# Optimization experiments

Measured on AMD Instinct MI355X. Metric: run time of the kernel, lower is better.

The kernel has to match this reference:

```python
import jax, jax.numpy as jnp
import numpy as np

RAD2DEG = 180.0 / 3.14159  # module uses 3.14159, not pi

def _conv2d(x, w):
    # x: (N,1,H,W), w: (O,1,3,3), SAME padding, stride 1
    return jax.lax.conv_general_dilated(
        x, w, window_strides=(1, 1), padding='SAME',
        dimension_numbers=('NCHW', 'OIHW', 'NCHW'))

def _make_filters():
    sobel = np.array([[1, 0, -1], [2, 0, -2], [1, 0, -1]], dtype=np.float32)
    f0   = [[0,0,0],[0,1,-1],[0,0,0]]
    f45  = [[0,0,0],[0,1,0],[0,0,-1]]
    f90  = [[0,0,0],[0,1,0],[0,-1,0]]
    f135 = [[0,0,0],[0,1,0],[-1,0,0]]
    f180 = [[0,0,0],[-1,1,0],[0,0,0]]
    f225 = [[-1,0,0],[0,1,0],[0,0,0]]
    f270 = [[0,-1,0],[0,1,0],[0,0,0]]
    f315 = [[0,0,-1],[0,1,0],[0,0,0]]
    dirs = np.stack([f0,f45,f90,f135,f180,f225,f270,f315]).astype(np.float32)
    return sobel, dirs

def setup_inputs() -> dict:
    key = jax.random.key(0)
    H, W = 2160, 3840
    img = jax.random.uniform(key, (1, 3, H, W), dtype=jnp.float32)
    sobel, dirs = _make_filters()
    sobel_h = jnp.asarray(sobel)[None, None]          # (1,1,3,3)
    sobel_v = jnp.asarray(sobel.T)[None, None]        # (1,1,3,3)
    dir_w = jnp.asarray(dirs)[:, None]                # (8,1,3,3)
    return {"img": img, "sobel_h": sobel_h, "sobel_v": sobel_v, "dir_w": dir_w}

def reference(img, sobel_h, sobel_v, dir_w):
    # grayscale: mean of the 3 channels
    gray = (img[:, 0:1] + img[:, 1:2] + img[:, 2:3]) / 3.0        # (1,1,H,W)
    grad_x = _conv2d(gray, sobel_h)
    grad_y = _conv2d(gray, sobel_v)
    grad_mag = jnp.sqrt(grad_x ** 2 + grad_y ** 2)                # (1,1,H,W)
    # orientation in degrees, snapped to multiples of 45 (round-half-even, like torch.round)
    ori = jnp.round((jnp.arctan2(grad_y, grad_x) * RAD2DEG + 180.0) / 45.0)
    idx_pos = jnp.mod(ori, 8.0).astype(jnp.int32)                 # (1,1,H,W)
    idx_neg = jnp.mod(ori + 4.0, 8.0).astype(jnp.int32)
    all_filtered = _conv2d(grad_mag, dir_w)                       # (1,8,H,W)
    # per-pixel channel select (the flattened gather in the original)
    pos = jnp.take_along_axis(all_filtered, idx_pos, axis=1)      # (1,1,H,W)
    neg = jnp.take_along_axis(all_filtered, idx_neg, axis=1)
    is_max = jnp.minimum(pos, neg) > 0.0
    # in-place aliasing in the original: thin_edges/early_threshold alias grad_mag,
    # so the final binary map is: is_max AND (grad_mag >= 0.2)
    th = jnp.where(is_max & (grad_mag >= 0.2), 1.0, 0.0).astype(jnp.float32)
    return th
```

## Files before the change

kernel.cpp:

```cpp
#include <hip/hip_runtime.h>
#include <math.h>

#define IMG_W 3840
#define IMG_H 2160
#define TW 128
#define TH 16

#define DXPACK 0x901A
#define DYPACK 0x1A9

#define T1_SLOPE 0.41421317376456f
#define T2_SLOPE 2.41420676743300f
#define SECT_EPS 3.0e-5f

__device__ __forceinline__ int slow_sector(float sx, float sy) {
#pragma clang fp contract(off)
    const float RADF = (float)(180.0 / 3.14159);
    float t = atan2f(sy, sx);
    float wv = ((t * RADF) + 180.0f) / 45.0f;
    float ori = rintf(wv);
    float fr = fabsf(wv - ori);
    if (fr > 0.4995f) {
        double td = atan2((double)sy, (double)sx);
        float t2 = (float)td;
        wv = ((t2 * RADF) + 180.0f) / 45.0f;
        ori = rintf(wv);
    }
    return ((int)ori) & 7;
}

__global__ __launch_bounds__(256) void canny_like_kernel(const float* __restrict__ img,
                                                         float* __restrict__ out) {
#pragma clang fp contract(off)
    __shared__ float lds_g[TH + 4][TW + 4];
    __shared__ float lds_m[TH + 2][TW + 2];

    const int tx = threadIdx.x;
    const int ty = threadIdx.y;
    const int tid = ty * TW + tx;
    const int x0 = blockIdx.x * TW;
    const int y0 = blockIdx.y * TH;

    for (int i = tid; i < (TH + 4) * (TW + 4); i += 256) {
        int ry = i / (TW + 4);
        int rx = i - ry * (TW + 4);
        int gyy = y0 - 2 + ry;
        int gxx = x0 - 2 + rx;
        float v = 0.0f;
        if (gyy >= 0 && gyy < IMG_H && gxx >= 0 && gxx < IMG_W) {
            int base = gyy * IMG_W + gxx;
            float c0 = img[base];
            float c1 = img[base + IMG_H * IMG_W];
            float c2 = img[base + 2 * IMG_H * IMG_W];
            v = ((c0 + c1) + c2) / 3.0f;
        }
        lds_g[ry][rx] = v;
    }
    __syncthreads();

    for (int i = tid; i < (TH + 2) * (TW + 2); i += 256) {
        int my = i / (TW + 2);
        int mx = i - my * (TW + 2);
        int gyy = y0 - 1 + my;
        int gxx = x0 - 1 + mx;
        float v = 0.0f;
        if (gyy >= 0 && gyy < IMG_H && gxx >= 0 && gxx < IMG_W) {
            float a00 = lds_g[my][mx],     a01 = lds_g[my][mx + 1],     a02 = lds_g[my][mx + 2];
            float a10 = lds_g[my + 1][mx],                              a12 = lds_g[my + 1][mx + 2];
            float a20 = lds_g[my + 2][mx], a21 = lds_g[my + 2][mx + 1], a22 = lds_g[my + 2][mx + 2];
            float sx = a00;
            sx = sx - a02;
            sx = sx + 2.0f * a10;
            sx = sx - 2.0f * a12;
            sx = sx + a20;
            sx = sx - a22;
            float sy = a00;
            sy = sy + 2.0f * a01;
            sy = sy + a02;
            sy = sy - a20;
            sy = sy - 2.0f * a21;
            sy = sy - a22;
            v = sqrtf(sx * sx + sy * sy);
        }
        lds_m[my][mx] = v;
    }
    __syncthreads();

    for (int r = 0; r < TH / 2; ++r) {
        int oy = r * 2 + ty;
        int my = oy + 1, mx = tx + 1;
        int ry = oy + 2, rx = tx + 2;
        float a00 = lds_g[ry - 1][rx - 1], a01 = lds_g[ry - 1][rx], a02 = lds_g[ry - 1][rx + 1];
        float a10 = lds_g[ry][rx - 1],                              a12 = lds_g[ry][rx + 1];
        float a20 = lds_g[ry + 1][rx - 1], a21 = lds_g[ry + 1][rx], a22 = lds_g[ry + 1][rx + 1];
        float sx = a00;
        sx = sx - a02;
        sx = sx + 2.0f * a10;
        sx = sx - 2.0f * a12;
        sx = sx + a20;
        sx = sx - a22;
        float sy = a00;
        sy = sy + 2.0f * a01;
        sy = sy + a02;
        sy = sy - a20;
        sy = sy - 2.0f * a21;
        sy = sy - a22;

        float ax = fabsf(sx), ay = fabsf(sy);
        float d1 = ay - T1_SLOPE * ax;
        float d2 = ay - T2_SLOPE * ax;
        float s = ax + ay;
        int idx;
        if (fabsf(d1) < SECT_EPS * s || fabsf(d2) < SECT_EPS * s) {
            idx = slow_sector(sx, sy);
        } else if (d1 < 0.0f) {
            idx = (sx > 0.0f) ? 4 : 0;
        } else if (d2 > 0.0f) {
            idx = (sy > 0.0f) ? 6 : 2;
        } else {
            idx = (sx > 0.0f) ? ((sy > 0.0f) ? 5 : 3)
                              : ((sy > 0.0f) ? 7 : 1);
        }
        int dxo = ((DXPACK >> (2 * idx)) & 3) - 1;
        int dyo = ((DYPACK >> (2 * idx)) & 3) - 1;

        float mc = lds_m[my][mx];
        float pos = mc - lds_m[my + dyo][mx + dxo];
        float neg = mc - lds_m[my - dyo][mx - dxo];
        float res = (fminf(pos, neg) > 0.0f && mc >= 0.2f) ? 1.0f : 0.0f;
        out[(y0 + oy) * IMG_W + (x0 + tx)] = res;
    }
}

extern "C" void kernel_launch(void* const* d_in, const int* in_sizes, int n_in,
                              void* d_out, int out_size, void* d_ws, size_t ws_size,
                              hipStream_t stream) {
    const float* img = (const float*)d_in[0];
    float* out = (float*)d_out;
    dim3 grid(IMG_W / TW, IMG_H / TH);
    dim3 block(TW, 2);
    canny_like_kernel<<<grid, block, 0, stream>>>(img, out);
}
```

Baseline: 178.5 us.

## Use overlapping tiles, compute orientation once per halo pixel, store neighbor offsets in LDS

Each block now loads a 128-wide tile that overlaps its neighbours by the halo and writes only the 124 inner output columns. Staging loops therefore map one thread to one column with no integer division. The gradient direction is computed once alongside the magnitude and stored as a packed LDS offset, so the final pass no longer recomputes the Sobel and reads neighbours through a single offset. slow_sector is marked noinline to keep register pressure down. In exchange, some halo work is redundant, the grid grows (31 column tiles with a partial last tile), and the final pass leaves a few lanes idle.

```diff
diff --git a/kernel.cpp b/kernel.cpp
--- a/kernel.cpp
+++ b/kernel.cpp
@@ -3,8 +3,11 @@
 
 #define IMG_W 3840
 #define IMG_H 2160
-#define TW 128
+#define TW 124
 #define TH 16
+#define LW 128
+#define GROWS (TH + 4)
+#define MROWS (TH + 2)
 
 #define DXPACK 0x901A
 #define DYPACK 0x1A9
@@ -13,7 +16,7 @@
 #define T2_SLOPE 2.41420676743300f
 #define SECT_EPS 3.0e-5f
 
-__device__ __forceinline__ int slow_sector(float sx, float sy) {
+__device__ __noinline__ int slow_sector(float sx, float sy) {
 #pragma clang fp contract(off)
     const float RADF = (float)(180.0 / 3.14159);
     float t = atan2f(sy, sx);
@@ -32,103 +35,88 @@
 __global__ __launch_bounds__(256) void canny_like_kernel(const float* __restrict__ img,
                                                          float* __restrict__ out) {
 #pragma clang fp contract(off)
-    __shared__ float lds_g[TH + 4][TW + 4];
-    __shared__ float lds_m[TH + 2][TW + 2];
+    __shared__ float lds_g[GROWS][LW];
+    __shared__ float lds_m[MROWS][LW];
+    __shared__ short lds_o[MROWS][LW];
 
-    const int tx = threadIdx.x;
-    const int ty = threadIdx.y;
-    const int tid = ty * TW + tx;
-    const int x0 = blockIdx.x * TW;
-    const int y0 = blockIdx.y * TH;
+    const int c = threadIdx.x;
+    const int h = threadIdx.y;
+    const int gx = blockIdx.x * TW - 2 + c;
+    const int gy0 = blockIdx.y * TH - 2;
+    const bool xok = (unsigned)gx < (unsigned)IMG_W;
 
-    for (int i = tid; i < (TH + 4) * (TW + 4); i += 256) {
-        int ry = i / (TW + 4);
-        int rx = i - ry * (TW + 4);
-        int gyy = y0 - 2 + ry;
-        int gxx = x0 - 2 + rx;
+    const float* p = img + gx;
+    for (int i = 0; i < GROWS / 2; ++i) {
+        int gy = gy0 + 2 * i + h;
         float v = 0.0f;
-        if (gyy >= 0 && gyy < IMG_H && gxx >= 0 && gxx < IMG_W) {
-            int base = gyy * IMG_W + gxx;
-            float c0 = img[base];
-            float c1 = img[base + IMG_H * IMG_W];
-            float c2 = img[base + 2 * IMG_H * IMG_W];
+        if (xok && (unsigned)gy < (unsigned)IMG_H) {
+            long o = (long)gy * IMG_W;
+            float c0 = p[o];
+            float c1 = p[o + (long)IMG_W * IMG_H];
+            float c2 = p[o + 2l * IMG_W * IMG_H];
             v = ((c0 + c1) + c2) / 3.0f;
         }
-        lds_g[ry][rx] = v;
+        lds_g[2 * i + h][c] = v;
     }
     __syncthreads();
 
-    for (int i = tid; i < (TH + 2) * (TW + 2); i += 256) {
-        int my = i / (TW + 2);
-        int mx = i - my * (TW + 2);
-        int gyy = y0 - 1 + my;
-        int gxx = x0 - 1 + mx;
-        float v = 0.0f;
-        if (gyy >= 0 && gyy < IMG_H && gxx >= 0 && gxx < IMG_W) {
-            float a00 = lds_g[my][mx],     a01 = lds_g[my][mx + 1],     a02 = lds_g[my][mx + 2];
-            float a10 = lds_g[my + 1][mx],                              a12 = lds_g[my + 1][mx + 2];
-            float a20 = lds_g[my + 2][mx], a21 = lds_g[my + 2][mx + 1], a22 = lds_g[my + 2][mx + 2];
-            float sx = a00;
-            sx = sx - a02;
-            sx = sx + 2.0f * a10;
-            sx = sx - 2.0f * a12;
-            sx = sx + a20;
-            sx = sx - a22;
-            float sy = a00;
-            sy = sy + 2.0f * a01;
-            sy = sy + a02;
-            sy = sy - a20;
-            sy = sy - 2.0f * a21;
-            sy = sy - a22;
-            v = sqrtf(sx * sx + sy * sy);
+    if (c >= 1 && c <= 126) {
+        for (int i = 0; i < MROWS / 2; ++i) {
+            int r = 2 * i + h;
+            int gy = gy0 + 1 + r;
+            float mag = 0.0f;
+            short offp = 0;
+            if (xok && (unsigned)gy < (unsigned)IMG_H) {
+                float a00 = lds_g[r][c - 1],     a01 = lds_g[r][c],     a02 = lds_g[r][c + 1];
+                float a10 = lds_g[r + 1][c - 1],                        a12 = lds_g[r + 1][c + 1];
+                float a20 = lds_g[r + 2][c - 1], a21 = lds_g[r + 2][c], a22 = lds_g[r + 2][c + 1];
+                float sx = a00;
+                sx = sx - a02;
+                sx = sx + 2.0f * a10;
+                sx = sx - 2.0f * a12;
+                sx = sx + a20;
+                sx = sx - a22;
+                float sy = a00;
+                sy = sy + 2.0f * a01;
+                sy = sy + a02;
+                sy = sy - a20;
+                sy = sy - 2.0f * a21;
+                sy = sy - a22;
+                mag = sqrtf(sx * sx + sy * sy);
+
+                float ax = fabsf(sx), ay = fabsf(sy);
+                float d1 = fmaf(-T1_SLOPE, ax, ay);
+                float d2 = fmaf(-T2_SLOPE, ax, ay);
+                float s = ax + ay;
+                int dxo, dyo;
+                if (fabsf(d1) < SECT_EPS * s || fabsf(d2) < SECT_EPS * s) {
+                    int idx = slow_sector(sx, sy);
+                    dxo = ((DXPACK >> (2 * idx)) & 3) - 1;
+                    dyo = ((DYPACK >> (2 * idx)) & 3) - 1;
+                } else {
+                    dxo = (d2 > 0.0f) ? 0 : ((sx > 0.0f) ? -1 : 1);
+                    dyo = (d1 < 0.0f) ? 0 : ((sy > 0.0f) ? -1 : 1);
+                }
+                offp = (short)(dyo * LW + dxo);
+            }
+            lds_m[r][c] = mag;
+            lds_o[r][c] = offp;
         }
-        lds_m[my][mx] = v;
     }
     __syncthreads();
 
-    for (int r = 0; r < TH / 2; ++r) {
-        int oy = r * 2 + ty;
-        int my = oy + 1, mx = tx + 1;
-        int ry = oy + 2, rx = tx + 2;
-        float a00 = lds_g[ry - 1][rx - 1], a01 = lds_g[ry - 1][rx], a02 = lds_g[ry - 1][rx + 1];
-        float a10 = lds_g[ry][rx - 1],                              a12 = lds_g[ry][rx + 1];
-        float a20 = lds_g[ry + 1][rx - 1], a21 = lds_g[ry + 1][rx], a22 = lds_g[ry + 1][rx + 1];
-        float sx = a00;
-        sx = sx - a02;
-        sx = sx + 2.0f * a10;
-        sx = sx - 2.0f * a12;
-        sx = sx + a20;
-        sx = sx - a22;
-        float sy = a00;
-        sy = sy + 2.0f * a01;
-        sy = sy + a02;
-        sy = sy - a20;
-        sy = sy - 2.0f * a21;
-        sy = sy - a22;
-
-        float ax = fabsf(sx), ay = fabsf(sy);
-        float d1 = ay - T1_SLOPE * ax;
-        float d2 = ay - T2_SLOPE * ax;
-        float s = ax + ay;
-        int idx;
-        if (fabsf(d1) < SECT_EPS * s || fabsf(d2) < SECT_EPS * s) {
-            idx = slow_sector(sx, sy);
-        } else if (d1 < 0.0f) {
-            idx = (sx > 0.0f) ? 4 : 0;
-        } else if (d2 > 0.0f) {
-            idx = (sy > 0.0f) ? 6 : 2;
-        } else {
-            idx = (sx > 0.0f) ? ((sy > 0.0f) ? 5 : 3)
-                              : ((sy > 0.0f) ? 7 : 1);
+    if (c >= 2 && c <= 125 && xok) {
+        for (int i = 0; i < TH / 2; ++i) {
+            int oy = 2 * i + h;
+            int mr = oy + 1;
+            float mc = lds_m[mr][c];
+            int off = lds_o[mr][c];
+            const float* mb = &lds_m[mr][c];
+            float mp = mb[off];
+            float mn = mb[-off];
+            float res = (fminf(mc - mp, mc - mn) > 0.0f && mc >= 0.2f) ? 1.0f : 0.0f;
+            out[(long)(gy0 + 2 + oy) * IMG_W + gx] = res;
         }
-        int dxo = ((DXPACK >> (2 * idx)) & 3) - 1;
-        int dyo = ((DYPACK >> (2 * idx)) & 3) - 1;
-
-        float mc = lds_m[my][mx];
-        float pos = mc - lds_m[my + dyo][mx + dxo];
-        float neg = mc - lds_m[my - dyo][mx - dxo];
-        float res = (fminf(pos, neg) > 0.0f && mc >= 0.2f) ? 1.0f : 0.0f;
-        out[(y0 + oy) * IMG_W + (x0 + tx)] = res;
     }
 }
 
@@ -137,7 +125,7 @@
                               hipStream_t stream) {
     const float* img = (const float*)d_in[0];
     float* out = (float*)d_out;
-    dim3 grid(IMG_W / TW, IMG_H / TH);
-    dim3 block(TW, 2);
+    dim3 grid((IMG_W + TW - 1) / TW, IMG_H / TH);
+    dim3 block(LW, 2);
     canny_like_kernel<<<grid, block, 0, stream>>>(img, out);
 }
```

Result: faster. 172.6 us (-3.3%).
